# Kernel optimization log

Hardware: AMD Instinct MI355X
Metric: run time of the kernel (lower is better)

Reference implementation:

```python
import jax, jax.numpy as jnp
import numpy as np

FP8_E4M3_MAX = 448.0
BLOCK = 32
EPS = 1e-30


def _quantize_fp8(blocks):
    # blocks: (..., num_blocks, BLOCK) float32
    max_abs = jnp.max(jnp.abs(blocks), axis=-1)                      # (..., nb)
    scales = jnp.maximum(max_abs / FP8_E4M3_MAX, EPS)                # shared fp32 scale per block
    fp8 = (blocks / scales[..., None]).astype(jnp.float8_e4m3fn).astype(jnp.float32)
    return fp8, scales


def setup_inputs() -> dict:
    key = jax.random.key(0)
    k1, k2, k3 = jax.random.split(key, 3)
    x = jax.random.normal(k1, (2048, 2048), dtype=jnp.float32)
    weight = jax.random.normal(k2, (2048, 2048), dtype=jnp.float32) * 0.02
    bias = jax.random.normal(k3, (2048,), dtype=jnp.float32) * 0.02
    return {"x": x, "weight": weight, "bias": bias}


def reference(x, weight, bias):
    N, in_f = x.shape
    out_f = weight.shape[0]
    nb = in_f // BLOCK  # in_features is a multiple of BLOCK, so no padding needed

    x_fp8, x_scales = _quantize_fp8(x.reshape(N, nb, BLOCK))         # (N, nb, B), (N, nb)
    w_fp8, w_scales = _quantize_fp8(weight.reshape(out_f, nb, BLOCK))  # (out, nb, B), (out, nb)

    # per-block fp8-element dot products: (nb, N, out)
    elem_dots = jnp.einsum('nbk,jbk->bnj', x_fp8, w_fp8)
    # apply shared block scales and reduce over blocks: out[n,j] = sum_b sx[n,b]*sw[j,b]*dots[b,n,j]
    result = jnp.einsum('bnj,nb,jb->nj', elem_dots, x_scales, w_scales)
    return result + bias
```

## Files before the change

kernel.cpp:

```cpp
#include <hip/hip_runtime.h>
#include <hip/hip_bf16.h>


typedef __attribute__((ext_vector_type(8))) __bf16 bf16x8;
typedef __attribute__((ext_vector_type(4))) float f32x4;

#define NMAT 2048
#define FP8_MAX 448.0f

__device__ inline unsigned short bfbits(float f) {
  union { __hip_bfloat16 h; unsigned short u; } cv;
  cv.h = __float2bfloat16(f);
  return cv.u;
}

__device__ inline unsigned pack2(float a, float b, float scale) {
  int p = __builtin_amdgcn_cvt_pk_fp8_f32(a / scale, b / scale, 0, false);
  float qa = __builtin_amdgcn_cvt_f32_fp8(p, 0) * scale;
  float qb = __builtin_amdgcn_cvt_f32_fp8(p, 1) * scale;
  return (unsigned)bfbits(qa) | ((unsigned)bfbits(qb) << 16);
}

__global__ __launch_bounds__(256) void qdq_kernel(const float* __restrict__ x,
                                                  uint2* __restrict__ xo,
                                                  const float* __restrict__ w,
                                                  uint2* __restrict__ wo) {
  int g = blockIdx.x;
  const float* in;
  uint2* out;
  if (g >= 4096) { in = w; out = wo; g -= 4096; }
  else           { in = x; out = xo; }
  const int t = threadIdx.x;
  const size_t base = (size_t)g * 1024;
  float4 v = ((const float4*)(in + base))[t];
  float amax = fmaxf(fmaxf(fabsf(v.x), fabsf(v.y)), fmaxf(fabsf(v.z), fabsf(v.w)));
  amax = fmaxf(amax, __shfl_xor(amax, 1));
  amax = fmaxf(amax, __shfl_xor(amax, 2));
  amax = fmaxf(amax, __shfl_xor(amax, 4));
  float scale = fmaxf(amax / FP8_MAX, 1e-30f);
  uint2 r;
  r.x = pack2(v.x, v.y, scale);
  r.y = pack2(v.z, v.w, scale);
  out[base / 4 + t] = r;
}

__global__ __launch_bounds__(256) void gemm_kernel(const __bf16* __restrict__ A,
                                                   const __bf16* __restrict__ B,
                                                   const float* __restrict__ bias,
                                                   float* __restrict__ C) {
  __shared__ __align__(16) char lds[49152];
  const int tid  = threadIdx.x;
  const int lane = tid & 63;
  const int wid  = tid >> 6;
  const int wr   = wid >> 1;
  const int wc   = wid & 1;

  const int bid = blockIdx.x;
  const int xcd = bid & 7;
  const int k8  = bid >> 3;
  const int tr  = (xcd >> 2) * 8 + (k8 >> 3);
  const int tc  = (xcd & 3) * 8 + (k8 & 7);
  const int row0 = tr * 128;
  const int col0 = tc * 64;

  int rS[4], cS[4];
#pragma unroll
  for (int i = 0; i < 4; ++i) {
    const int o = i * 4096 + tid * 16;
    rS[i] = o >> 7;
    cS[i] = (o & 127) ^ ((rS[i] & 7) << 4);
  }
  const char* AgS[4];
  const char* BgS[2];
#pragma unroll
  for (int i = 0; i < 4; ++i)
    AgS[i] = (const char*)A + (size_t)(row0 + rS[i]) * 4096 + cS[i];
#pragma unroll
  for (int j = 0; j < 2; ++j)
    BgS[j] = (const char*)B + (size_t)(col0 + rS[j]) * 4096 + cS[j];
  const int dst = tid * 16;

#define STAGE(buf, kt) do {                                                      \
    const int kb = (kt) * 128;                                                   \
    char* lb = lds + (buf) * 24576;                                              \
    _Pragma("unroll")                                                            \
    for (int i = 0; i < 4; ++i)                                                  \
      __builtin_amdgcn_global_load_lds(                                          \
          (const __attribute__((address_space(1))) unsigned*)(AgS[i] + kb),      \
          (__attribute__((address_space(3))) unsigned*)(lb + i * 4096 + dst),    \
          16, 0, 0);                                                             \
    _Pragma("unroll")                                                            \
    for (int j = 0; j < 2; ++j)                                                  \
      __builtin_amdgcn_global_load_lds(                                          \
          (const __attribute__((address_space(1))) unsigned*)(BgS[j] + kb),      \
          (__attribute__((address_space(3))) unsigned*)(lb + 16384 + j * 4096 + dst), \
          16, 0, 0);                                                             \
  } while (0)

#define WAIT6_BAR() do {                                   \
    asm volatile("s_waitcnt vmcnt(6)" ::: "memory");       \
    __builtin_amdgcn_sched_barrier(0);                     \
    __builtin_amdgcn_s_barrier();                          \
  } while (0)
#define POST_BAR() do {                                    \
    __builtin_amdgcn_sched_barrier(0);                     \
    __builtin_amdgcn_s_barrier();                          \
  } while (0)

  const int l15 = lane & 15;
  const int q16 = (lane >> 4) * 16;
  const int swz = (l15 & 7) << 4;
  const int ck0 = q16 ^ swz;
  const int ck1 = (64 + q16) ^ swz;
  const int aRow = (wr * 64 + l15) * 128;
  const int bRow = (wc * 32 + l15) * 128;

  f32x4 acc[4][2] = {};

  auto compute = [&](const int buf) {
    const char* ab = lds + buf * 24576;
    const char* bb = ab + 16384;
    bf16x8 a0[4], a1[4], b0[2], b1[2];
#pragma unroll
    for (int m = 0; m < 4; ++m) {
      a0[m] = *(const bf16x8*)(ab + aRow + m * 2048 + ck0);
      a1[m] = *(const bf16x8*)(ab + aRow + m * 2048 + ck1);
    }
#pragma unroll
    for (int n = 0; n < 2; ++n) {
      b0[n] = *(const bf16x8*)(bb + bRow + n * 2048 + ck0);
      b1[n] = *(const bf16x8*)(bb + bRow + n * 2048 + ck1);
    }
#pragma unroll
    for (int m = 0; m < 4; ++m)
#pragma unroll
      for (int n = 0; n < 2; ++n) {
        acc[m][n] = __builtin_amdgcn_mfma_f32_16x16x32_bf16(a0[m], b0[n], acc[m][n], 0, 0, 0);
        acc[m][n] = __builtin_amdgcn_mfma_f32_16x16x32_bf16(a1[m], b1[n], acc[m][n], 0, 0, 0);
      }
  };

  STAGE(0, 0);
#pragma unroll 1
  for (int t = 0; t < 30; t += 2) {
    STAGE(1, t + 1);
    WAIT6_BAR();
    compute(0);
    POST_BAR();
    STAGE(0, t + 2);
    WAIT6_BAR();
    compute(1);
    POST_BAR();
  }
  STAGE(1, 31);
  WAIT6_BAR();
  compute(0);
  POST_BAR();
  asm volatile("s_waitcnt vmcnt(0)" ::: "memory");
  __builtin_amdgcn_sched_barrier(0);
  __builtin_amdgcn_s_barrier();
  compute(1);

  const int rb = row0 + wr * 64 + (lane >> 4) * 4;
#pragma unroll
  for (int n = 0; n < 2; ++n) {
    const int j = col0 + wc * 32 + n * 16 + l15;
    const float bv = bias[j];
#pragma unroll
    for (int m = 0; m < 4; ++m)
#pragma unroll
      for (int r = 0; r < 4; ++r)
        C[(size_t)(rb + m * 16 + r) * NMAT + j] = acc[m][n][r] + bv;
  }
#undef STAGE
#undef WAIT6_BAR
#undef POST_BAR
}

extern "C" void kernel_launch(void* const* d_in, const int* in_sizes, int n_in,
                              void* d_out, int out_size, void* d_ws, size_t ws_size,
                              hipStream_t stream) {
  const float* x  = (const float*)d_in[0];
  const float* w  = (const float*)d_in[1];
  const float* bs = (const float*)d_in[2];
  float* out = (float*)d_out;

  uint2* xd = (uint2*)d_ws;
  uint2* wd = xd + (NMAT * (size_t)NMAT / 4);

  qdq_kernel<<<dim3(8192), dim3(256), 0, stream>>>(x, xd, w, wd);

  gemm_kernel<<<dim3(512), dim3(256), 0, stream>>>((const __bf16*)xd,
                                                   (const __bf16*)wd, bs, out);
}
```

Measured before the change: 104.4 us.

## Store FP8 bytes plus block scales and dequantize to bf16 inside GEMM

The quantize kernel now writes packed FP8 bytes, permuted within each 64-element chunk, and one fp32 scale per 32-element block, where before it wrote fully dequantized bf16. The GEMM stages FP8 and scale tiles through LDS and converts them to scaled bf16 in registers right before the MFMAs. This halves the intermediate tensors written and read from global memory and shrinks the LDS footprint. In exchange it adds per-tile conversion ALU work to the GEMM inner loop and issues small 4-byte LDS-direct loads for the scales.

```diff
diff --git a/kernel.cpp b/kernel.cpp
--- a/kernel.cpp
+++ b/kernel.cpp
@@ -4,32 +4,27 @@
 
 typedef __attribute__((ext_vector_type(8))) __bf16 bf16x8;
 typedef __attribute__((ext_vector_type(4))) float f32x4;
+typedef __attribute__((ext_vector_type(2))) float f32x2;
 
 #define NMAT 2048
 #define FP8_MAX 448.0f
 
-__device__ inline unsigned short bfbits(float f) {
-  union { __hip_bfloat16 h; unsigned short u; } cv;
+__device__ inline __bf16 tobf(float f) {
+  union { __hip_bfloat16 h; __bf16 b; } cv;
   cv.h = __float2bfloat16(f);
-  return cv.u;
-}
-
-__device__ inline unsigned pack2(float a, float b, float scale) {
-  int p = __builtin_amdgcn_cvt_pk_fp8_f32(a / scale, b / scale, 0, false);
-  float qa = __builtin_amdgcn_cvt_f32_fp8(p, 0) * scale;
-  float qb = __builtin_amdgcn_cvt_f32_fp8(p, 1) * scale;
-  return (unsigned)bfbits(qa) | ((unsigned)bfbits(qb) << 16);
+  return cv.b;
 }
 
 __global__ __launch_bounds__(256) void qdq_kernel(const float* __restrict__ x,
-                                                  uint2* __restrict__ xo,
+                                                  unsigned char* __restrict__ xq,
+                                                  float* __restrict__ xs,
                                                   const float* __restrict__ w,
-                                                  uint2* __restrict__ wo) {
+                                                  unsigned char* __restrict__ wq,
+                                                  float* __restrict__ wss) {
   int g = blockIdx.x;
-  const float* in;
-  uint2* out;
-  if (g >= 4096) { in = w; out = wo; g -= 4096; }
-  else           { in = x; out = xo; }
+  const float* in; unsigned char* oq; float* os;
+  if (g >= 4096) { in = w; oq = wq; os = wss; g -= 4096; }
+  else           { in = x; oq = xq; os = xs; }
   const int t = threadIdx.x;
   const size_t base = (size_t)g * 1024;
   float4 v = ((const float4*)(in + base))[t];
@@ -37,18 +32,48 @@
   amax = fmaxf(amax, __shfl_xor(amax, 1));
   amax = fmaxf(amax, __shfl_xor(amax, 2));
   amax = fmaxf(amax, __shfl_xor(amax, 4));
-  float scale = fmaxf(amax / FP8_MAX, 1e-30f);
-  uint2 r;
-  r.x = pack2(v.x, v.y, scale);
-  r.y = pack2(v.z, v.w, scale);
-  out[base / 4 + t] = r;
-}
-
-__global__ __launch_bounds__(256) void gemm_kernel(const __bf16* __restrict__ A,
-                                                   const __bf16* __restrict__ B,
+  float s = fmaxf(amax / FP8_MAX, 1e-30f);
+  int p = __builtin_amdgcn_cvt_pk_fp8_f32(v.x / s, v.y / s, 0, false);
+  p = __builtin_amdgcn_cvt_pk_fp8_f32(v.z / s, v.w / s, p, true);
+  const int idx = (int)base + t * 4;
+  const int row = idx >> 11;
+  const int k = idx & 2047;
+  const int pb = (k & ~63) | (((k >> 3) & 3) << 4) | (((k >> 5) & 1) << 3) | (k & 7);
+  *(unsigned*)(oq + (size_t)row * 2048 + pb) = (unsigned)p;
+  if ((t & 7) == 0) os[row * 64 + (k >> 5)] = s;
+}
+
+__device__ inline bf16x8 dq8(unsigned w0, unsigned w1, float s) {
+  bf16x8 r;
+#if __has_builtin(__builtin_amdgcn_cvt_pk_f32_fp8)
+  f32x2 p01 = __builtin_amdgcn_cvt_pk_f32_fp8((int)w0, false);
+  f32x2 p23 = __builtin_amdgcn_cvt_pk_f32_fp8((int)w0, true);
+  f32x2 p45 = __builtin_amdgcn_cvt_pk_f32_fp8((int)w1, false);
+  f32x2 p67 = __builtin_amdgcn_cvt_pk_f32_fp8((int)w1, true);
+  r[0] = tobf(p01[0] * s); r[1] = tobf(p01[1] * s);
+  r[2] = tobf(p23[0] * s); r[3] = tobf(p23[1] * s);
+  r[4] = tobf(p45[0] * s); r[5] = tobf(p45[1] * s);
+  r[6] = tobf(p67[0] * s); r[7] = tobf(p67[1] * s);
+#else
+  r[0] = tobf(__builtin_amdgcn_cvt_f32_fp8((int)w0, 0) * s);
+  r[1] = tobf(__builtin_amdgcn_cvt_f32_fp8((int)w0, 1) * s);
+  r[2] = tobf(__builtin_amdgcn_cvt_f32_fp8((int)w0, 2) * s);
+  r[3] = tobf(__builtin_amdgcn_cvt_f32_fp8((int)w0, 3) * s);
+  r[4] = tobf(__builtin_amdgcn_cvt_f32_fp8((int)w1, 0) * s);
+  r[5] = tobf(__builtin_amdgcn_cvt_f32_fp8((int)w1, 1) * s);
+  r[6] = tobf(__builtin_amdgcn_cvt_f32_fp8((int)w1, 2) * s);
+  r[7] = tobf(__builtin_amdgcn_cvt_f32_fp8((int)w1, 3) * s);
+#endif
+  return r;
+}
+
+__global__ __launch_bounds__(256) void gemm_kernel(const unsigned char* __restrict__ Aq,
+                                                   const float* __restrict__ As,
+                                                   const unsigned char* __restrict__ Bq,
+                                                   const float* __restrict__ Bs,
                                                    const float* __restrict__ bias,
                                                    float* __restrict__ C) {
-  __shared__ __align__(16) char lds[49152];
+  __shared__ __align__(16) char lds[28672];
   const int tid  = threadIdx.x;
   const int lane = tid & 63;
   const int wid  = tid >> 6;
@@ -58,47 +83,38 @@
   const int bid = blockIdx.x;
   const int xcd = bid & 7;
   const int k8  = bid >> 3;
-  const int tr  = (xcd >> 2) * 8 + (k8 >> 3);
-  const int tc  = (xcd & 3) * 8 + (k8 & 7);
-  const int row0 = tr * 128;
-  const int col0 = tc * 64;
-
-  int rS[4], cS[4];
-#pragma unroll
-  for (int i = 0; i < 4; ++i) {
-    const int o = i * 4096 + tid * 16;
-    rS[i] = o >> 7;
-    cS[i] = (o & 127) ^ ((rS[i] & 7) << 4);
-  }
-  const char* AgS[4];
-  const char* BgS[2];
-#pragma unroll
-  for (int i = 0; i < 4; ++i)
-    AgS[i] = (const char*)A + (size_t)(row0 + rS[i]) * 4096 + cS[i];
-#pragma unroll
-  for (int j = 0; j < 2; ++j)
-    BgS[j] = (const char*)B + (size_t)(col0 + rS[j]) * 4096 + cS[j];
-  const int dst = tid * 16;
+  const int row0 = ((xcd >> 2) * 8 + (k8 >> 3)) * 128;
+  const int col0 = ((xcd & 3) * 8 + (k8 & 7)) * 64;
+
+  const unsigned char* AgD0 = Aq + (size_t)(row0 + (tid >> 2)) * 2048 + (tid & 3) * 16;
+  const unsigned char* AgD1 = Aq + (size_t)(row0 + 64 + (tid >> 2)) * 2048 + (tid & 3) * 16;
+  const unsigned char* BgD  = Bq + (size_t)(col0 + (tid >> 2)) * 2048 + (tid & 3) * 16;
+  const float* AgS = As + (size_t)(row0 + (tid >> 1)) * 64 + (tid & 1);
+  const float* BgS = Bs + (size_t)(col0 + ((tid & 127) >> 1)) * 64 + (tid & 1);
+  const int dst16 = tid * 16;
+  const int dst4  = tid * 4;
 
 #define STAGE(buf, kt) do {                                                      \
-    const int kb = (kt) * 128;                                                   \
-    char* lb = lds + (buf) * 24576;                                              \
-    _Pragma("unroll")                                                            \
-    for (int i = 0; i < 4; ++i)                                                  \
-      __builtin_amdgcn_global_load_lds(                                          \
-          (const __attribute__((address_space(1))) unsigned*)(AgS[i] + kb),      \
-          (__attribute__((address_space(3))) unsigned*)(lb + i * 4096 + dst),    \
-          16, 0, 0);                                                             \
-    _Pragma("unroll")                                                            \
-    for (int j = 0; j < 2; ++j)                                                  \
-      __builtin_amdgcn_global_load_lds(                                          \
-          (const __attribute__((address_space(1))) unsigned*)(BgS[j] + kb),      \
-          (__attribute__((address_space(3))) unsigned*)(lb + 16384 + j * 4096 + dst), \
-          16, 0, 0);                                                             \
+    char* lb = lds + (buf) * 14336;                                              \
+    __builtin_amdgcn_global_load_lds(                                            \
+        (const __attribute__((address_space(1))) unsigned*)(AgD0 + (kt) * 64),   \
+        (__attribute__((address_space(3))) unsigned*)(lb + dst16), 16, 0, 0);    \
+    __builtin_amdgcn_global_load_lds(                                            \
+        (const __attribute__((address_space(1))) unsigned*)(AgD1 + (kt) * 64),   \
+        (__attribute__((address_space(3))) unsigned*)(lb + 4096 + dst16), 16, 0, 0); \
+    __builtin_amdgcn_global_load_lds(                                            \
+        (const __attribute__((address_space(1))) unsigned*)(BgD + (kt) * 64),    \
+        (__attribute__((address_space(3))) unsigned*)(lb + 8192 + dst16), 16, 0, 0); \
+    __builtin_amdgcn_global_load_lds(                                            \
+        (const __attribute__((address_space(1))) unsigned*)(AgS + (kt) * 2),     \
+        (__attribute__((address_space(3))) unsigned*)(lb + 12288 + dst4), 4, 0, 0);  \
+    __builtin_amdgcn_global_load_lds(                                            \
+        (const __attribute__((address_space(1))) unsigned*)(BgS + (kt) * 2),     \
+        (__attribute__((address_space(3))) unsigned*)(lb + 13312 + dst4), 4, 0, 0);  \
   } while (0)
 
-#define WAIT6_BAR() do {                                   \
-    asm volatile("s_waitcnt vmcnt(6)" ::: "memory");       \
+#define WAIT5_BAR() do {                                   \
+    asm volatile("s_waitcnt vmcnt(5)" ::: "memory");       \
     __builtin_amdgcn_sched_barrier(0);                     \
     __builtin_amdgcn_s_barrier();                          \
   } while (0)
@@ -108,28 +124,36 @@
   } while (0)
 
   const int l15 = lane & 15;
-  const int q16 = (lane >> 4) * 16;
-  const int swz = (l15 & 7) << 4;
-  const int ck0 = q16 ^ swz;
-  const int ck1 = (64 + q16) ^ swz;
-  const int aRow = (wr * 64 + l15) * 128;
-  const int bRow = (wc * 32 + l15) * 128;
+  const int lq  = (lane >> 4) * 16;
 
   f32x4 acc[4][2] = {};
 
   auto compute = [&](const int buf) {
-    const char* ab = lds + buf * 24576;
-    const char* bb = ab + 16384;
+    const char* lb = lds + buf * 14336;
+    uint4 araw[4]; f32x2 ascl[4];
+    uint4 braw[2]; f32x2 bscl[2];
+#pragma unroll
+    for (int m = 0; m < 4; ++m) {
+      const int r = wr * 64 + m * 16 + l15;
+      araw[m] = *(const uint4*)(lb + r * 64 + lq);
+      ascl[m] = *(const f32x2*)(lb + 12288 + r * 8);
+    }
+#pragma unroll
+    for (int n = 0; n < 2; ++n) {
+      const int r = wc * 32 + n * 16 + l15;
+      braw[n] = *(const uint4*)(lb + 8192 + r * 64 + lq);
+      bscl[n] = *(const f32x2*)(lb + 13312 + r * 8);
+    }
     bf16x8 a0[4], a1[4], b0[2], b1[2];
 #pragma unroll
     for (int m = 0; m < 4; ++m) {
-      a0[m] = *(const bf16x8*)(ab + aRow + m * 2048 + ck0);
-      a1[m] = *(const bf16x8*)(ab + aRow + m * 2048 + ck1);
+      a0[m] = dq8(araw[m].x, araw[m].y, ascl[m][0]);
+      a1[m] = dq8(araw[m].z, araw[m].w, ascl[m][1]);
     }
 #pragma unroll
     for (int n = 0; n < 2; ++n) {
-      b0[n] = *(const bf16x8*)(bb + bRow + n * 2048 + ck0);
-      b1[n] = *(const bf16x8*)(bb + bRow + n * 2048 + ck1);
+      b0[n] = dq8(braw[n].x, braw[n].y, bscl[n][0]);
+      b1[n] = dq8(braw[n].z, braw[n].w, bscl[n][1]);
     }
 #pragma unroll
     for (int m = 0; m < 4; ++m)
@@ -144,16 +168,16 @@
 #pragma unroll 1
   for (int t = 0; t < 30; t += 2) {
     STAGE(1, t + 1);
-    WAIT6_BAR();
+    WAIT5_BAR();
     compute(0);
     POST_BAR();
     STAGE(0, t + 2);
-    WAIT6_BAR();
+    WAIT5_BAR();
     compute(1);
     POST_BAR();
   }
   STAGE(1, 31);
-  WAIT6_BAR();
+  WAIT5_BAR();
   compute(0);
   POST_BAR();
   asm volatile("s_waitcnt vmcnt(0)" ::: "memory");
@@ -173,7 +197,7 @@
         C[(size_t)(rb + m * 16 + r) * NMAT + j] = acc[m][n][r] + bv;
   }
 #undef STAGE
-#undef WAIT6_BAR
+#undef WAIT5_BAR
 #undef POST_BAR
 }
 
@@ -185,11 +209,12 @@
   const float* bs = (const float*)d_in[2];
   float* out = (float*)d_out;
 
-  uint2* xd = (uint2*)d_ws;
-  uint2* wd = xd + (NMAT * (size_t)NMAT / 4);
-
-  qdq_kernel<<<dim3(8192), dim3(256), 0, stream>>>(x, xd, w, wd);
-
-  gemm_kernel<<<dim3(512), dim3(256), 0, stream>>>((const __bf16*)xd,
-                                                   (const __bf16*)wd, bs, out);
-}
+  unsigned char* xq = (unsigned char*)d_ws;
+  unsigned char* wq = xq + 4u * 1024 * 1024;
+  float* xs  = (float*)(xq + 8u * 1024 * 1024);
+  float* wss = xs + 2048 * 64;
+
+  qdq_kernel<<<dim3(8192), dim3(256), 0, stream>>>(x, xq, xs, w, wq, wss);
+
+  gemm_kernel<<<dim3(512), dim3(256), 0, stream>>>(xq, xs, wq, wss, bs, out);
+}
```

New measurement: 137.0 us. +31.2%, slower.
